# Optimization experiments

Hardware: AMD Instinct MI355X
Metric: run time of the kernel (lower is better)

Reference implementation:

```python
import jax, jax.numpy as jnp
import numpy as np

B, S, DM = 4, 8192, 1024
N_RED = 16384   # tokens merged into their right neighbor
N_SAVE = 16384  # tokens kept; must be divisible by B


def setup_inputs() -> dict:
    key = jax.random.key(0)
    k1, k2, k3, k4 = jax.random.split(key, 4)
    x = jax.random.normal(k1, (B, S, DM), dtype=jnp.float32)
    W = jax.random.normal(k2, (DM, DM), dtype=jnp.float32) * (1.0 / np.sqrt(DM))
    ids_to_reduce = jax.random.randint(k3, (N_RED,), 0, B * S - 1, dtype=jnp.int64)
    ids_to_save = jax.random.randint(k4, (N_SAVE,), 0, B * S, dtype=jnp.int64)
    return {"x": x, "W": W, "ids_to_save": ids_to_save, "ids_to_reduce": ids_to_reduce}


def reference(x, W, ids_to_save, ids_to_reduce):
    batch_size, _, dm = x.shape
    xf = x.reshape(-1, dm)                       # [B*S, dm]
    reduced = xf[ids_to_reduce]                  # gather  [N_RED, dm]
    transformed = (reduced @ W.T).astype(jnp.float32)  # Linear, no bias
    xf = xf.at[ids_to_reduce + 1].add(transformed)     # scatter-add into right neighbor
    saved = xf[ids_to_save]                      # gather  [N_SAVE, dm]
    return saved.reshape(batch_size, -1, dm)     # [B, N_SAVE//B, dm]
```

## Files before the change

kernel.cpp:

```cpp
#include <hip/hip_runtime.h>

#define DM    1024
#define NTOK  32768
#define NRED  16384
#define NSAVE 16384
#define MMAX  16384

typedef __attribute__((ext_vector_type(8))) short bf16x8;
typedef __attribute__((ext_vector_type(4))) float f32x4;

__device__ __forceinline__ ushort f2bf(float f) {
    union { float f; unsigned u; } v; v.f = f;
    unsigned r = (v.u + 0x7FFF + ((v.u >> 16) & 1)) >> 16;
    return (ushort)r;
}
__device__ __forceinline__ float bf2f(ushort u) {
    union { unsigned u; float f; } v; v.u = ((unsigned)u) << 16;
    return v.f;
}

__global__ __launch_bounds__(256) void setup_kernel(const float* __restrict__ W,
                                                    ushort* __restrict__ Wb,
                                                    int* __restrict__ cnt,
                                                    int* __restrict__ need,
                                                    int* __restrict__ counter) {
    int t = blockIdx.x * 256 + threadIdx.x;
    float4 v = ((const float4*)W)[t];
    ushort4 o;
    o.x = f2bf(v.x); o.y = f2bf(v.y); o.z = f2bf(v.z); o.w = f2bf(v.w);
    ((ushort4*)Wb)[t] = o;
    if (t < NTOK) { cnt[t] = 0; need[t] = 0; }
    if (t == 0) *counter = 0;
}

__global__ __launch_bounds__(256) void prep_kernel(const int* __restrict__ red,
                                                   const int* __restrict__ sav,
                                                   int* __restrict__ cnt,
                                                   int* __restrict__ need) {
    int j = blockIdx.x * 256 + threadIdx.x;
    if (j >= NRED) return;
    atomicAdd(&cnt[red[j]], 1);
    int s = sav[j];
    if (s > 0) need[s - 1] = 1;
}

__global__ __launch_bounds__(256) void compact_kernel(const int* __restrict__ cnt,
                                                      const int* __restrict__ need,
                                                      int* __restrict__ inv,
                                                      int* __restrict__ list,
                                                      int* __restrict__ counter) {
    int t = blockIdx.x * 256 + threadIdx.x;
    if (t >= NTOK) return;
    if (need[t] && cnt[t] > 0) {
        int pos = atomicAdd(counter, 1);
        inv[t] = pos;
        list[pos] = t;
    }
}

__global__ __launch_bounds__(256) void convx_kernel(const float* __restrict__ X,
                                                    const int* __restrict__ list,
                                                    const int* __restrict__ counter,
                                                    ushort* __restrict__ Xb) {
    const int M = *counter;
    const int Mpad = (M + 63) & ~63;
    for (int r = blockIdx.x; r < Mpad; r += gridDim.x) {
        ushort4 o;
        if (r < M) {
            int src = list[r];
            float4 v = ((const float4*)(X + (size_t)src * DM))[threadIdx.x];
            o.x = f2bf(v.x); o.y = f2bf(v.y); o.z = f2bf(v.z); o.w = f2bf(v.w);
        } else {
            o.x = 0; o.y = 0; o.z = 0; o.w = 0;
        }
        ((ushort4*)(Xb + (size_t)r * DM))[threadIdx.x] = o;
    }
}

__global__ __launch_bounds__(64) void gemm_kernel(const ushort* __restrict__ Xb,
                                                  const ushort* __restrict__ Wb,
                                                  const int* __restrict__ counter,
                                                  ushort* __restrict__ Tb) {
    const int M = *counter;
    const int m0 = blockIdx.x * 64;
    if (m0 >= M) return;
    const int n0 = blockIdx.y * 64;

    __shared__ char lds[32768];

    const int l = threadIdx.x;
    const int srow   = l >> 3;
    const int schunk = (l & 7) ^ (srow & 7);
    const ushort* aS = Xb + (size_t)(m0 + srow) * DM + schunk * 8;
    const ushort* bS = Wb + (size_t)(n0 + srow) * DM + schunk * 8;

#define STAGE(buf, k0) do {                                                         \
    char* _d = lds + (buf) * 16384;                                                 \
    _Pragma("unroll")                                                               \
    for (int _i = 0; _i < 8; ++_i) {                                                \
        __builtin_amdgcn_global_load_lds(                                           \
            (const __attribute__((address_space(1))) unsigned*)(aS + (k0) + _i * 8 * DM), \
            (__attribute__((address_space(3))) unsigned*)(_d + _i * 1024), 16, 0, 0);     \
        __builtin_amdgcn_global_load_lds(                                           \
            (const __attribute__((address_space(1))) unsigned*)(bS + (k0) + _i * 8 * DM), \
            (__attribute__((address_space(3))) unsigned*)(_d + 8192 + _i * 1024), 16, 0, 0); \
    }                                                                               \
} while (0)

    const int kgrp = l >> 4;
    const int r16  = l & 15;
    int off[4][2];
#pragma unroll
    for (int f = 0; f < 4; ++f) {
        int row = f * 16 + r16;
#pragma unroll
        for (int kk = 0; kk < 2; ++kk)
            off[f][kk] = row * 128 + (((kk * 4 + kgrp) ^ (row & 7)) * 16);
    }

    f32x4 acc[4][4] = {};

    STAGE(0, 0);
#pragma unroll
    for (int t = 0; t < 16; ++t) {
        const char* base = lds + (t & 1) * 16384;
        if (t < 15) {
            asm volatile("s_waitcnt lgkmcnt(0)" ::: "memory");
            __builtin_amdgcn_sched_barrier(0);
            STAGE((t & 1) ^ 1, (t + 1) * 64);
            asm volatile("s_waitcnt vmcnt(16)" ::: "memory");
            __builtin_amdgcn_sched_barrier(0);
        } else {
            asm volatile("s_waitcnt vmcnt(0)" ::: "memory");
            __builtin_amdgcn_sched_barrier(0);
        }
#pragma unroll
        for (int kk = 0; kk < 2; ++kk) {
            bf16x8 af[4], bfr[4];
#pragma unroll
            for (int f = 0; f < 4; ++f) af[f]  = *(const bf16x8*)(base + off[f][kk]);
#pragma unroll
            for (int f = 0; f < 4; ++f) bfr[f] = *(const bf16x8*)(base + 8192 + off[f][kk]);
#pragma unroll
            for (int i = 0; i < 4; ++i)
#pragma unroll
                for (int j = 0; j < 4; ++j)
                    acc[i][j] = __builtin_amdgcn_mfma_f32_16x16x32_bf16(af[i], bfr[j], acc[i][j], 0, 0, 0);
        }
    }
#undef STAGE

#pragma unroll
    for (int fm = 0; fm < 4; ++fm) {
        int mbase = m0 + fm * 16 + kgrp * 4;
#pragma unroll
        for (int fn = 0; fn < 4; ++fn) {
            int n = n0 + fn * 16 + r16;
#pragma unroll
            for (int r = 0; r < 4; ++r) {
                int m = mbase + r;
                if (m < M) Tb[(size_t)m * DM + n] = f2bf(acc[fm][fn][r]);
            }
        }
    }
}

__global__ __launch_bounds__(256) void out_kernel(const float* __restrict__ X,
                                                  const ushort* __restrict__ Tb,
                                                  const int* __restrict__ sav,
                                                  const int* __restrict__ cnt,
                                                  const int* __restrict__ inv,
                                                  float* __restrict__ out) {
    int r = blockIdx.x;
    int d = threadIdx.x;
    int s = sav[r];
    const float4* xr = (const float4*)(X + (size_t)s * DM);
    float4 v = xr[d];
    if (s > 0) {
        int t = s - 1;
        int c = cnt[t];
        if (c > 0) {
            float fc = (float)c;
            const ushort4* tr = (const ushort4*)(Tb + (size_t)inv[t] * DM);
            ushort4 wv = tr[d];
            v.x += fc * bf2f(wv.x); v.y += fc * bf2f(wv.y);
            v.z += fc * bf2f(wv.z); v.w += fc * bf2f(wv.w);
        }
    }
    ((float4*)out)[(size_t)r * (DM / 4) + d] = v;
}

extern "C" void kernel_launch(void* const* d_in, const int* in_sizes, int n_in,
                              void* d_out, int out_size, void* d_ws, size_t ws_size,
                              hipStream_t stream) {
    const float* X   = (const float*)d_in[0];
    const float* W   = (const float*)d_in[1];
    const int*   sav = (const int*)d_in[2];
    const int*   red = (const int*)d_in[3];
    float* out = (float*)d_out;

    char* ws = (char*)d_ws;
    int* counter = (int*)ws;
    int* cnt  = counter + 64;
    int* need = cnt + NTOK;
    int* inv  = need + NTOK;
    int* list = inv + NTOK;
    ushort* Wb = (ushort*)(ws + (1 << 19));
    ushort* Xb = (ushort*)(ws + (4 << 20));
    ushort* Tb = (ushort*)(ws + (36u << 20));

    setup_kernel<<<DM * DM / 4 / 256, 256, 0, stream>>>(W, Wb, cnt, need, counter);
    prep_kernel<<<NRED / 256, 256, 0, stream>>>(red, sav, cnt, need);
    compact_kernel<<<NTOK / 256, 256, 0, stream>>>(cnt, need, inv, list, counter);
    convx_kernel<<<2048, 256, 0, stream>>>(X, list, counter, Xb);

    dim3 ggrid(MMAX / 64, DM / 64);
    gemm_kernel<<<ggrid, 64, 0, stream>>>(Xb, Wb, counter, Tb);

    out_kernel<<<NSAVE, 256, 0, stream>>>(X, Tb, sav, cnt, inv, out);
}
```

Measured before the change: 76.49 us.

## Enlarge GEMM tile to 128x128 with four cooperating waves sharing LDS

Changes the bf16 GEMM from 64x64 tiles on a single wave to 128x128 tiles on 256 threads. Each wave computes 32 rows against all 128 columns and loads a quarter of the shared A/B stages, with block barriers around the double-buffered LDS. This raises operand reuse and reduces global and LDS traffic per MFMA. In exchange it adds workgroup barriers, uses 64KB of LDS per block, and launches fewer blocks. Padding of M is raised to a multiple of 128 to match the new tile.

Result: faster. 67.34 us (-12.0%).

```diff
diff --git a/kernel.cpp b/kernel.cpp
--- a/kernel.cpp
+++ b/kernel.cpp
@@ -63,7 +63,7 @@
                                                     const int* __restrict__ counter,
                                                     ushort* __restrict__ Xb) {
     const int M = *counter;
-    const int Mpad = (M + 63) & ~63;
+    const int Mpad = (M + 127) & ~127;
     for (int r = blockIdx.x; r < Mpad; r += gridDim.x) {
         ushort4 o;
         if (r < M) {
@@ -77,84 +77,97 @@
     }
 }
 
-__global__ __launch_bounds__(64) void gemm_kernel(const ushort* __restrict__ Xb,
-                                                  const ushort* __restrict__ Wb,
-                                                  const int* __restrict__ counter,
-                                                  ushort* __restrict__ Tb) {
+__global__ __launch_bounds__(256) void gemm_kernel(const ushort* __restrict__ Xb,
+                                                   const ushort* __restrict__ Wb,
+                                                   const int* __restrict__ counter,
+                                                   ushort* __restrict__ Tb) {
     const int M = *counter;
-    const int m0 = blockIdx.x * 64;
+    const int m0 = blockIdx.x * 128;
     if (m0 >= M) return;
-    const int n0 = blockIdx.y * 64;
-
-    __shared__ char lds[32768];
-
-    const int l = threadIdx.x;
+    const int n0 = blockIdx.y * 128;
+
+    __shared__ char lds[65536];
+
+    const int tid  = threadIdx.x;
+    const int l    = tid & 63;
+    const int w    = tid >> 6;
+
     const int srow   = l >> 3;
     const int schunk = (l & 7) ^ (srow & 7);
-    const ushort* aS = Xb + (size_t)(m0 + srow) * DM + schunk * 8;
-    const ushort* bS = Wb + (size_t)(n0 + srow) * DM + schunk * 8;
-
-#define STAGE(buf, k0) do {                                                         \
-    char* _d = lds + (buf) * 16384;                                                 \
-    _Pragma("unroll")                                                               \
-    for (int _i = 0; _i < 8; ++_i) {                                                \
-        __builtin_amdgcn_global_load_lds(                                           \
+    const ushort* aS = Xb + (size_t)(m0 + w * 32 + srow) * DM + schunk * 8;
+    const ushort* bS = Wb + (size_t)(n0 + w * 32 + srow) * DM + schunk * 8;
+    const int dOff   = (w * 32) * 128;
+
+#define STAGE(buf, k0) do {                                                          \
+    char* _a = lds + (buf) * 32768 + dOff;                                           \
+    _Pragma("unroll")                                                                \
+    for (int _i = 0; _i < 4; ++_i) {                                                 \
+        __builtin_amdgcn_global_load_lds(                                            \
             (const __attribute__((address_space(1))) unsigned*)(aS + (k0) + _i * 8 * DM), \
-            (__attribute__((address_space(3))) unsigned*)(_d + _i * 1024), 16, 0, 0);     \
-        __builtin_amdgcn_global_load_lds(                                           \
+            (__attribute__((address_space(3))) unsigned*)(_a + _i * 1024), 16, 0, 0);      \
+        __builtin_amdgcn_global_load_lds(                                            \
             (const __attribute__((address_space(1))) unsigned*)(bS + (k0) + _i * 8 * DM), \
-            (__attribute__((address_space(3))) unsigned*)(_d + 8192 + _i * 1024), 16, 0, 0); \
-    }                                                                               \
+            (__attribute__((address_space(3))) unsigned*)(_a + 16384 + _i * 1024), 16, 0, 0); \
+    }                                                                                \
 } while (0)
 
     const int kgrp = l >> 4;
     const int r16  = l & 15;
-    int off[4][2];
-#pragma unroll
-    for (int f = 0; f < 4; ++f) {
-        int row = f * 16 + r16;
+    int aoff[2][2], boff[8][2];
+#pragma unroll
+    for (int fm = 0; fm < 2; ++fm) {
+        int row = w * 32 + fm * 16 + r16;
 #pragma unroll
         for (int kk = 0; kk < 2; ++kk)
-            off[f][kk] = row * 128 + (((kk * 4 + kgrp) ^ (row & 7)) * 16);
-    }
-
-    f32x4 acc[4][4] = {};
+            aoff[fm][kk] = row * 128 + (((kk * 4 + kgrp) ^ (row & 7)) * 16);
+    }
+#pragma unroll
+    for (int fn = 0; fn < 8; ++fn) {
+        int row = fn * 16 + r16;
+#pragma unroll
+        for (int kk = 0; kk < 2; ++kk)
+            boff[fn][kk] = 16384 + row * 128 + (((kk * 4 + kgrp) ^ (row & 7)) * 16);
+    }
+
+    f32x4 acc[2][8] = {};
 
     STAGE(0, 0);
 #pragma unroll
     for (int t = 0; t < 16; ++t) {
-        const char* base = lds + (t & 1) * 16384;
+        const char* base = lds + (t & 1) * 32768;
         if (t < 15) {
-            asm volatile("s_waitcnt lgkmcnt(0)" ::: "memory");
-            __builtin_amdgcn_sched_barrier(0);
             STAGE((t & 1) ^ 1, (t + 1) * 64);
-            asm volatile("s_waitcnt vmcnt(16)" ::: "memory");
-            __builtin_amdgcn_sched_barrier(0);
+            asm volatile("s_waitcnt vmcnt(8)" ::: "memory");
         } else {
             asm volatile("s_waitcnt vmcnt(0)" ::: "memory");
-            __builtin_amdgcn_sched_barrier(0);
-        }
+        }
+        __builtin_amdgcn_sched_barrier(0);
+        __builtin_amdgcn_s_barrier();
+
 #pragma unroll
         for (int kk = 0; kk < 2; ++kk) {
-            bf16x8 af[4], bfr[4];
-#pragma unroll
-            for (int f = 0; f < 4; ++f) af[f]  = *(const bf16x8*)(base + off[f][kk]);
-#pragma unroll
-            for (int f = 0; f < 4; ++f) bfr[f] = *(const bf16x8*)(base + 8192 + off[f][kk]);
-#pragma unroll
-            for (int i = 0; i < 4; ++i)
-#pragma unroll
-                for (int j = 0; j < 4; ++j)
-                    acc[i][j] = __builtin_amdgcn_mfma_f32_16x16x32_bf16(af[i], bfr[j], acc[i][j], 0, 0, 0);
-        }
+            bf16x8 af[2], bfr[8];
+#pragma unroll
+            for (int fm = 0; fm < 2; ++fm) af[fm]  = *(const bf16x8*)(base + aoff[fm][kk]);
+#pragma unroll
+            for (int fn = 0; fn < 8; ++fn) bfr[fn] = *(const bf16x8*)(base + boff[fn][kk]);
+#pragma unroll
+            for (int fm = 0; fm < 2; ++fm)
+#pragma unroll
+                for (int fn = 0; fn < 8; ++fn)
+                    acc[fm][fn] = __builtin_amdgcn_mfma_f32_16x16x32_bf16(af[fm], bfr[fn], acc[fm][fn], 0, 0, 0);
+        }
+
+        if (t < 15)
+            __builtin_amdgcn_s_barrier();
     }
 #undef STAGE
 
 #pragma unroll
-    for (int fm = 0; fm < 4; ++fm) {
-        int mbase = m0 + fm * 16 + kgrp * 4;
-#pragma unroll
-        for (int fn = 0; fn < 4; ++fn) {
+    for (int fm = 0; fm < 2; ++fm) {
+        int mbase = m0 + w * 32 + fm * 16 + kgrp * 4;
+#pragma unroll
+        for (int fn = 0; fn < 8; ++fn) {
             int n = n0 + fn * 16 + r16;
 #pragma unroll
             for (int r = 0; r < 4; ++r) {
@@ -214,8 +227,8 @@
     compact_kernel<<<NTOK / 256, 256, 0, stream>>>(cnt, need, inv, list, counter);
     convx_kernel<<<2048, 256, 0, stream>>>(X, list, counter, Xb);
 
-    dim3 ggrid(MMAX / 64, DM / 64);
-    gemm_kernel<<<ggrid, 64, 0, stream>>>(Xb, Wb, counter, Tb);
+    dim3 ggrid(MMAX / 128, DM / 128);
+    gemm_kernel<<<ggrid, 256, 0, stream>>>(Xb, Wb, counter, Tb);
 
     out_kernel<<<NSAVE, 256, 0, stream>>>(X, Tb, sav, cnt, inv, out);
 }
```

## Rewrite GEMM with 256x256 tiles, 8 waves, and split-K partials

Applied to the files above, without the earlier changes.

The GEMM moves from 64x64 tiles on one wave to 256x256 tiles on 8 waves, using 128KB of double-buffered LDS. It also adds split-K by 2 along blockIdx.z, and each half writes its own bf16 partial buffer. Loads, barriers and MFMA groups are interleaved in quarter steps, with setprio raised around the MFMAs. out_kernel now sums the two partials. The aim is better data reuse and more MFMA throughput, at the cost of doubling the intermediate writes and reads and rounding each partial to bf16.

Result: faster. 71.58 us (-6.4%).

```diff
diff --git a/kernel.cpp b/kernel.cpp
--- a/kernel.cpp
+++ b/kernel.cpp
@@ -5,6 +5,8 @@
 #define NRED  16384
 #define NSAVE 16384
 #define MMAX  16384
+#define AS1 __attribute__((address_space(1)))
+#define AS3 __attribute__((address_space(3)))
 
 typedef __attribute__((ext_vector_type(8))) short bf16x8;
 typedef __attribute__((ext_vector_type(4))) float f32x4;
@@ -63,7 +65,7 @@
                                                     const int* __restrict__ counter,
                                                     ushort* __restrict__ Xb) {
     const int M = *counter;
-    const int Mpad = (M + 63) & ~63;
+    const int Mpad = (M + 255) & ~255;
     for (int r = blockIdx.x; r < Mpad; r += gridDim.x) {
         ushort4 o;
         if (r < M) {
@@ -77,96 +79,193 @@
     }
 }
 
-__global__ __launch_bounds__(64) void gemm_kernel(const ushort* __restrict__ Xb,
-                                                  const ushort* __restrict__ Wb,
-                                                  const int* __restrict__ counter,
-                                                  ushort* __restrict__ Tb) {
+__global__ __launch_bounds__(512) void gemm_kernel(const ushort* __restrict__ Xb,
+                                                   const ushort* __restrict__ Wb,
+                                                   const int* __restrict__ counter,
+                                                   ushort* __restrict__ Tp) {
     const int M = *counter;
-    const int m0 = blockIdx.x * 64;
+    const int m0 = blockIdx.x * 256;
     if (m0 >= M) return;
-    const int n0 = blockIdx.y * 64;
-
-    __shared__ char lds[32768];
-
-    const int l = threadIdx.x;
-    const int srow   = l >> 3;
-    const int schunk = (l & 7) ^ (srow & 7);
-    const ushort* aS = Xb + (size_t)(m0 + srow) * DM + schunk * 8;
-    const ushort* bS = Wb + (size_t)(n0 + srow) * DM + schunk * 8;
-
-#define STAGE(buf, k0) do {                                                         \
-    char* _d = lds + (buf) * 16384;                                                 \
-    _Pragma("unroll")                                                               \
-    for (int _i = 0; _i < 8; ++_i) {                                                \
-        __builtin_amdgcn_global_load_lds(                                           \
-            (const __attribute__((address_space(1))) unsigned*)(aS + (k0) + _i * 8 * DM), \
-            (__attribute__((address_space(3))) unsigned*)(_d + _i * 1024), 16, 0, 0);     \
-        __builtin_amdgcn_global_load_lds(                                           \
-            (const __attribute__((address_space(1))) unsigned*)(bS + (k0) + _i * 8 * DM), \
-            (__attribute__((address_space(3))) unsigned*)(_d + 8192 + _i * 1024), 16, 0, 0); \
-    }                                                                               \
+    const int n0 = blockIdx.y * 256;
+    const int kw = blockIdx.z;
+    ushort* Tout = Tp + (size_t)kw * ((size_t)MMAX * DM);
+
+    extern __shared__ char lds[];
+
+    const int tid = threadIdx.x;
+    const int l   = tid & 63;
+    const int wid = tid >> 6;
+    const int wr  = wid >> 2;
+    const int wn  = wid & 3;
+    const int tr  = tid >> 3;
+    const int ch  = (tid & 7) ^ (tr & 7);
+
+    const ushort* aP0 = Xb + (size_t)(m0 + tr) * DM + ch * 8;
+    const ushort* aP1 = aP0 + (size_t)128 * DM;
+    const int brr = (tr < 32) ? tr : (tr + 32);
+    const ushort* bP0 = Wb + (size_t)(n0 + brr) * DM + ch * 8;
+    const ushort* bP1 = bP0 + (size_t)128 * DM;
+
+    const int adb = wid * 8 * 128;
+    const int bdb = 32768 + ((wid >> 2) * 64 + (wid & 3) * 8) * 128;
+
+#define STG_A(nb, h, kn) do {                                                         \
+    __builtin_amdgcn_global_load_lds((const AS1 unsigned*)(aP0 + (h) * 64 * DM + (kn)), \
+        (AS3 unsigned*)(lds + (nb) + adb + (h) * 8192), 16, 0, 0);                    \
+    __builtin_amdgcn_global_load_lds((const AS1 unsigned*)(aP1 + (h) * 64 * DM + (kn)), \
+        (AS3 unsigned*)(lds + (nb) + adb + 16384 + (h) * 8192), 16, 0, 0);            \
 } while (0)
-
-    const int kgrp = l >> 4;
-    const int r16  = l & 15;
-    int off[4][2];
-#pragma unroll
-    for (int f = 0; f < 4; ++f) {
-        int row = f * 16 + r16;
-#pragma unroll
-        for (int kk = 0; kk < 2; ++kk)
-            off[f][kk] = row * 128 + (((kk * 4 + kgrp) ^ (row & 7)) * 16);
-    }
-
-    f32x4 acc[4][4] = {};
-
-    STAGE(0, 0);
-#pragma unroll
-    for (int t = 0; t < 16; ++t) {
-        const char* base = lds + (t & 1) * 16384;
-        if (t < 15) {
+#define STG_B(nb, h, kn) do {                                                         \
+    __builtin_amdgcn_global_load_lds((const AS1 unsigned*)(bP0 + (h) * 32 * DM + (kn)), \
+        (AS3 unsigned*)(lds + (nb) + bdb + (h) * 4096), 16, 0, 0);                    \
+    __builtin_amdgcn_global_load_lds((const AS1 unsigned*)(bP1 + (h) * 32 * DM + (kn)), \
+        (AS3 unsigned*)(lds + (nb) + bdb + 16384 + (h) * 4096), 16, 0, 0);            \
+} while (0)
+
+    const int kg  = l >> 4;
+    const int r16 = l & 15;
+    const int c0 = ((kg ^ (r16 & 7)) << 4);
+    const int c1 = (((4 + kg) ^ (r16 & 7)) << 4);
+    int arb[8], brb[4];
+#pragma unroll
+    for (int f = 0; f < 8; ++f) arb[f] = (wr * 128 + f * 16 + r16) * 128;
+#pragma unroll
+    for (int f = 0; f < 4; ++f) brb[f] = 32768 + (wn * 64 + f * 16 + r16) * 128;
+
+    f32x4 acc[8][4] = {};
+    bf16x8 af[4][2];
+
+    const int kb = kw * 512;
+    STG_A(0, 0, kb); STG_B(0, 0, kb); STG_A(0, 1, kb); STG_B(0, 1, kb);
+
+#pragma unroll 2
+    for (int krel = 0; krel < 8; ++krel) {
+        const int cb = (krel & 1) * 65536;
+        const int nb = cb ^ 65536;
+        const int kn = kb + ((krel < 7) ? (krel + 1) : krel) * 64;
+
+        STG_A(nb, 0, kn);
+        asm volatile("s_waitcnt vmcnt(6)" ::: "memory");
+        __builtin_amdgcn_sched_barrier(0);
+        __builtin_amdgcn_s_barrier();
+        {
+            bf16x8 bf[2][2];
+#pragma unroll
+            for (int fm = 0; fm < 4; ++fm) {
+                af[fm][0] = *(const bf16x8*)(lds + cb + arb[fm] + c0);
+                af[fm][1] = *(const bf16x8*)(lds + cb + arb[fm] + c1);
+            }
+#pragma unroll
+            for (int fn = 0; fn < 2; ++fn) {
+                bf[fn][0] = *(const bf16x8*)(lds + cb + brb[fn] + c0);
+                bf[fn][1] = *(const bf16x8*)(lds + cb + brb[fn] + c1);
+            }
             asm volatile("s_waitcnt lgkmcnt(0)" ::: "memory");
             __builtin_amdgcn_sched_barrier(0);
-            STAGE((t & 1) ^ 1, (t + 1) * 64);
-            asm volatile("s_waitcnt vmcnt(16)" ::: "memory");
+            __builtin_amdgcn_s_setprio(1);
+#pragma unroll
+            for (int fm = 0; fm < 4; ++fm)
+#pragma unroll
+                for (int fn = 0; fn < 2; ++fn) {
+                    acc[fm][fn] = __builtin_amdgcn_mfma_f32_16x16x32_bf16(af[fm][0], bf[fn][0], acc[fm][fn], 0, 0, 0);
+                    acc[fm][fn] = __builtin_amdgcn_mfma_f32_16x16x32_bf16(af[fm][1], bf[fn][1], acc[fm][fn], 0, 0, 0);
+                }
+            __builtin_amdgcn_s_setprio(0);
+        }
+        STG_B(nb, 0, kn);
+        asm volatile("s_waitcnt vmcnt(4)" ::: "memory");
+        __builtin_amdgcn_sched_barrier(0);
+        __builtin_amdgcn_s_barrier();
+        {
+            bf16x8 bf[2][2];
+#pragma unroll
+            for (int fn = 0; fn < 2; ++fn) {
+                bf[fn][0] = *(const bf16x8*)(lds + cb + brb[2 + fn] + c0);
+                bf[fn][1] = *(const bf16x8*)(lds + cb + brb[2 + fn] + c1);
+            }
+            asm volatile("s_waitcnt lgkmcnt(0)" ::: "memory");
             __builtin_amdgcn_sched_barrier(0);
-        } else {
-            asm volatile("s_waitcnt vmcnt(0)" ::: "memory");
+            __builtin_amdgcn_s_setprio(1);
+#pragma unroll
+            for (int fm = 0; fm < 4; ++fm)
+#pragma unroll
+                for (int fn = 0; fn < 2; ++fn) {
+                    acc[fm][2 + fn] = __builtin_amdgcn_mfma_f32_16x16x32_bf16(af[fm][0], bf[fn][0], acc[fm][2 + fn], 0, 0, 0);
+                    acc[fm][2 + fn] = __builtin_amdgcn_mfma_f32_16x16x32_bf16(af[fm][1], bf[fn][1], acc[fm][2 + fn], 0, 0, 0);
+                }
+            __builtin_amdgcn_s_setprio(0);
+        }
+        STG_A(nb, 1, kn);
+        __builtin_amdgcn_sched_barrier(0);
+        __builtin_amdgcn_s_barrier();
+        {
+            bf16x8 bf[2][2];
+#pragma unroll
+            for (int fm = 0; fm < 4; ++fm) {
+                af[fm][0] = *(const bf16x8*)(lds + cb + arb[4 + fm] + c0);
+                af[fm][1] = *(const bf16x8*)(lds + cb + arb[4 + fm] + c1);
+            }
+#pragma unroll
+            for (int fn = 0; fn < 2; ++fn) {
+                bf[fn][0] = *(const bf16x8*)(lds + cb + brb[fn] + c0);
+                bf[fn][1] = *(const bf16x8*)(lds + cb + brb[fn] + c1);
+            }
+            asm volatile("s_waitcnt lgkmcnt(0)" ::: "memory");
             __builtin_amdgcn_sched_barrier(0);
-        }
-#pragma unroll
-        for (int kk = 0; kk < 2; ++kk) {
-            bf16x8 af[4], bfr[4];
-#pragma unroll
-            for (int f = 0; f < 4; ++f) af[f]  = *(const bf16x8*)(base + off[f][kk]);
-#pragma unroll
-            for (int f = 0; f < 4; ++f) bfr[f] = *(const bf16x8*)(base + 8192 + off[f][kk]);
-#pragma unroll
-            for (int i = 0; i < 4; ++i)
-#pragma unroll
-                for (int j = 0; j < 4; ++j)
-                    acc[i][j] = __builtin_amdgcn_mfma_f32_16x16x32_bf16(af[i], bfr[j], acc[i][j], 0, 0, 0);
-        }
-    }
-#undef STAGE
-
-#pragma unroll
-    for (int fm = 0; fm < 4; ++fm) {
-        int mbase = m0 + fm * 16 + kgrp * 4;
+            __builtin_amdgcn_s_setprio(1);
+#pragma unroll
+            for (int fm = 0; fm < 4; ++fm)
+#pragma unroll
+                for (int fn = 0; fn < 2; ++fn) {
+                    acc[4 + fm][fn] = __builtin_amdgcn_mfma_f32_16x16x32_bf16(af[fm][0], bf[fn][0], acc[4 + fm][fn], 0, 0, 0);
+                    acc[4 + fm][fn] = __builtin_amdgcn_mfma_f32_16x16x32_bf16(af[fm][1], bf[fn][1], acc[4 + fm][fn], 0, 0, 0);
+                }
+            __builtin_amdgcn_s_setprio(0);
+        }
+        STG_B(nb, 1, kn);
+        __builtin_amdgcn_sched_barrier(0);
+        __builtin_amdgcn_s_barrier();
+        {
+            bf16x8 bf[2][2];
+#pragma unroll
+            for (int fn = 0; fn < 2; ++fn) {
+                bf[fn][0] = *(const bf16x8*)(lds + cb + brb[2 + fn] + c0);
+                bf[fn][1] = *(const bf16x8*)(lds + cb + brb[2 + fn] + c1);
+            }
+            asm volatile("s_waitcnt lgkmcnt(0)" ::: "memory");
+            __builtin_amdgcn_sched_barrier(0);
+            __builtin_amdgcn_s_setprio(1);
+#pragma unroll
+            for (int fm = 0; fm < 4; ++fm)
+#pragma unroll
+                for (int fn = 0; fn < 2; ++fn) {
+                    acc[4 + fm][2 + fn] = __builtin_amdgcn_mfma_f32_16x16x32_bf16(af[fm][0], bf[fn][0], acc[4 + fm][2 + fn], 0, 0, 0);
+                    acc[4 + fm][2 + fn] = __builtin_amdgcn_mfma_f32_16x16x32_bf16(af[fm][1], bf[fn][1], acc[4 + fm][2 + fn], 0, 0, 0);
+                }
+            __builtin_amdgcn_s_setprio(0);
+        }
+    }
+    asm volatile("s_waitcnt vmcnt(0)" ::: "memory");
+#undef STG_A
+#undef STG_B
+
+#pragma unroll
+    for (int fm = 0; fm < 8; ++fm) {
+        int mbase = m0 + wr * 128 + fm * 16 + kg * 4;
 #pragma unroll
         for (int fn = 0; fn < 4; ++fn) {
-            int n = n0 + fn * 16 + r16;
+            int n = n0 + wn * 64 + fn * 16 + r16;
 #pragma unroll
             for (int r = 0; r < 4; ++r) {
                 int m = mbase + r;
-                if (m < M) Tb[(size_t)m * DM + n] = f2bf(acc[fm][fn][r]);
+                if (m < M) Tout[(size_t)m * DM + n] = f2bf(acc[fm][fn][r]);
             }
         }
     }
 }
 
 __global__ __launch_bounds__(256) void out_kernel(const float* __restrict__ X,
-                                                  const ushort* __restrict__ Tb,
+                                                  const ushort* __restrict__ Tp,
                                                   const int* __restrict__ sav,
                                                   const int* __restrict__ cnt,
                                                   const int* __restrict__ inv,
@@ -181,10 +280,13 @@
         int c = cnt[t];
         if (c > 0) {
             float fc = (float)c;
-            const ushort4* tr = (const ushort4*)(Tb + (size_t)inv[t] * DM);
-            ushort4 wv = tr[d];
-            v.x += fc * bf2f(wv.x); v.y += fc * bf2f(wv.y);
-            v.z += fc * bf2f(wv.z); v.w += fc * bf2f(wv.w);
+            size_t rowoff = (size_t)inv[t] * DM;
+            ushort4 p0 = ((const ushort4*)(Tp + rowoff))[d];
+            ushort4 p1 = ((const ushort4*)(Tp + (size_t)MMAX * DM + rowoff))[d];
+            v.x += fc * (bf2f(p0.x) + bf2f(p1.x));
+            v.y += fc * (bf2f(p0.y) + bf2f(p1.y));
+            v.z += fc * (bf2f(p0.z) + bf2f(p1.z));
+            v.w += fc * (bf2f(p0.w) + bf2f(p1.w));
         }
     }
     ((float4*)out)[(size_t)r * (DM / 4) + d] = v;
@@ -207,15 +309,15 @@
     int* list = inv + NTOK;
     ushort* Wb = (ushort*)(ws + (1 << 19));
     ushort* Xb = (ushort*)(ws + (4 << 20));
-    ushort* Tb = (ushort*)(ws + (36u << 20));
+    ushort* Tp = (ushort*)(ws + (36u << 20));
 
     setup_kernel<<<DM * DM / 4 / 256, 256, 0, stream>>>(W, Wb, cnt, need, counter);
     prep_kernel<<<NRED / 256, 256, 0, stream>>>(red, sav, cnt, need);
     compact_kernel<<<NTOK / 256, 256, 0, stream>>>(cnt, need, inv, list, counter);
     convx_kernel<<<2048, 256, 0, stream>>>(X, list, counter, Xb);
 
-    dim3 ggrid(MMAX / 64, DM / 64);
-    gemm_kernel<<<ggrid, 64, 0, stream>>>(Xb, Wb, counter, Tb);
-
-    out_kernel<<<NSAVE, 256, 0, stream>>>(X, Tb, sav, cnt, inv, out);
-}
+    dim3 ggrid(MMAX / 256, DM / 256, 2);
+    gemm_kernel<<<ggrid, 512, 131072, stream>>>(Xb, Wb, counter, Tp);
+
+    out_kernel<<<NSAVE, 256, 0, stream>>>(X, Tp, sav, cnt, inv, out);
+}
```
